# Kernel tuning notes

Hardware: AMD Instinct MI355X
Metric: run time of the kernel (lower is better)

## Reference

```python
import jax, jax.numpy as jnp
import numpy as np

N = 100000
E = 1600000
IN_FEATS = 512
N_CLASSES = 40
H1, D1 = 8, 8
H2, D2 = 1, N_CLASSES


def gat_conv(x, src, dst, W, al, ar, b, H, D):
    # x: [N, F] -> h: [N, H, D]
    n = x.shape[0]
    h = (x @ W).reshape(n, H, D)
    el = (h * al[None]).sum(-1)  # [N, H]
    er = (h * ar[None]).sum(-1)  # [N, H]
    e = jax.nn.leaky_relu(el[src] + er[dst], 0.2)  # [E, H]
    # segment softmax over destination neighborhoods
    emax = jax.ops.segment_max(e, dst, num_segments=n)  # [N, H]
    ee = jnp.exp(e - emax[dst])
    denom = jax.ops.segment_sum(ee, dst, num_segments=n)  # [N, H]
    a = ee / (denom[dst] + 1e-9)  # [E, H]
    m = h[src] * a[:, :, None]  # [E, H, D]
    out = jax.ops.segment_sum(m, dst, num_segments=n)  # [N, H, D]
    return out + b.reshape(1, H, D)


def setup_inputs() -> dict:
    key = jax.random.key(0)
    ks = jax.random.split(key, 12)
    g1 = 1.0 / np.sqrt(IN_FEATS)
    g2 = 1.0 / np.sqrt(H1 * D1)
    return {
        "x": jax.random.normal(ks[0], (N, IN_FEATS), jnp.float32),
        "src": jax.random.randint(ks[1], (E,), 0, N, jnp.int32),
        "dst": jax.random.randint(ks[2], (E,), 0, N, jnp.int32),
        "W1": jax.random.normal(ks[3], (IN_FEATS, H1 * D1), jnp.float32) * g1,
        "al1": jax.random.normal(ks[4], (H1, D1), jnp.float32) * 0.1,
        "ar1": jax.random.normal(ks[5], (H1, D1), jnp.float32) * 0.1,
        "b1": jnp.zeros((H1 * D1,), jnp.float32),
        "W2": jax.random.normal(ks[6], (H1 * D1, H2 * D2), jnp.float32) * g2,
        "al2": jax.random.normal(ks[7], (H2, D2), jnp.float32) * 0.1,
        "ar2": jax.random.normal(ks[8], (H2, D2), jnp.float32) * 0.1,
        "b2": jnp.zeros((H2 * D2,), jnp.float32),
    }


def reference(x, src, dst, W1, al1, ar1, b1, W2, al2, ar2, b2):
    h = gat_conv(x, src, dst, W1, al1, ar1, b1, H1, D1)  # [N, 8, 8]
    h = jax.nn.elu(h.reshape(N, H1 * D1))  # [N, 64]
    h = gat_conv(h, src, dst, W2, al2, ar2, b2, H2, D2).mean(axis=1)  # [N, n_classes]
    return jax.nn.log_softmax(h, axis=1)
```

## Files before the change

kernel.cpp:

```cpp
#include <hip/hip_runtime.h>
#include <hip/hip_bf16.h>
#include <math.h>

#define NCLS 40
#define H2S 64
#define PWG 256
#define BSH 9
#define NBMAX 512
#define SRCB 23
#define CSRCAP 14336

typedef __attribute__((ext_vector_type(8))) short bf16x8;
typedef __attribute__((ext_vector_type(4))) float f32x4;

__device__ inline float bf2f(ushort u) {
    unsigned v = ((unsigned)u) << 16;
    float f;
    __builtin_memcpy(&f, &v, 4);
    return f;
}
__device__ inline ushort f2bf(float f) {
    unsigned v;
    __builtin_memcpy(&v, &f, 4);
    unsigned r = (v + 0x7FFFu + ((v >> 16) & 1u)) >> 16;
    return (ushort)r;
}
__device__ inline unsigned pkbf(float a, float b) {
    unsigned ua, ub;
    __builtin_memcpy(&ua, &a, 4);
    __builtin_memcpy(&ub, &b, 4);
    return __builtin_amdgcn_perm(ub + 0x8000u, ua + 0x8000u, 0x07060302u);
}

__global__ __launch_bounds__(256) void hist_prep_kernel(
    const int* __restrict__ dst, int* __restrict__ hist, int Ee, int chunk, int NB,
    const float* __restrict__ W1, ushort* __restrict__ W1t,
    const float* __restrict__ W2, const float* __restrict__ al2,
    const float* __restrict__ ar2, float* __restrict__ wal2,
    float* __restrict__ war2)
{
    if (blockIdx.x >= PWG) {
        int bb = blockIdx.x - PWG;
        if (bb < 128) {
            int id = bb * 256 + threadIdx.x;
            int k = id >> 6, c = id & 63;
            W1t[c * 512 + k] = f2bf(W1[k * 64 + c]);
        } else if (threadIdx.x < 64) {
            int k = threadIdx.x;
            float a = 0.f, b = 0.f;
            for (int c = 0; c < NCLS; c++) {
                float w = W2[k * NCLS + c];
                a += w * al2[c];
                b += w * ar2[c];
            }
            wal2[k] = a;
            war2[k] = b;
        }
        return;
    }
    __shared__ int lh[256];
    const int wg = blockIdx.x, tid = threadIdx.x;
    lh[tid] = 0;
    __syncthreads();
    const int beg = wg * chunk;
    const int endv = min(Ee, beg + chunk);
#pragma unroll 4
    for (int i = beg + tid; i < endv; i += 256) atomicAdd(&lh[dst[i] >> BSH], 1);
    __syncthreads();
    if (tid < NB) hist[tid * PWG + wg] = lh[tid];
}

__global__ __launch_bounds__(256) void scanA_kernel(int* __restrict__ hist,
                                                    int* __restrict__ bucketTot)
{
    __shared__ int s[256];
    const int b = blockIdx.x, tid = threadIdx.x;
    int v = hist[b * PWG + tid];
    s[tid] = v;
    __syncthreads();
#pragma unroll
    for (int o = 1; o < 256; o <<= 1) {
        int t = (tid >= o) ? s[tid - o] : 0;
        __syncthreads();
        s[tid] += t;
        __syncthreads();
    }
    hist[b * PWG + tid] = s[tid] - v;
    if (tid == 255) bucketTot[b] = s[255];
}

__global__ __launch_bounds__(256) void part_gemm1_kernel(
    const int* __restrict__ src, const int* __restrict__ dst,
    const int* __restrict__ hist, const int* __restrict__ bucketTot,
    unsigned* __restrict__ ebuf, int Ee, int chunk, int NB,
    const float* __restrict__ x, const ushort* __restrict__ W1t,
    const float* __restrict__ al1, const float* __restrict__ ar1,
    ushort* __restrict__ h1b, float* __restrict__ el1,
    float* __restrict__ er1, int Nn)
{
    __shared__ ushort As[64 * 72];
    __shared__ ushort Bs[64 * 72];

    if (blockIdx.x < PWG) {
        int* cur = (int*)As;
        int* stmp = (int*)Bs;
        const int wg = blockIdx.x, tid = threadIdx.x;
        int v = (tid < NB) ? bucketTot[tid] : 0;
        stmp[tid] = v;
        __syncthreads();
#pragma unroll
        for (int o = 1; o < 256; o <<= 1) {
            int t = (tid >= o) ? stmp[tid - o] : 0;
            __syncthreads();
            stmp[tid] += t;
            __syncthreads();
        }
        if (tid < NB) cur[tid] = hist[tid * PWG + wg] + (stmp[tid] - v);
        __syncthreads();
        const int beg = wg * chunk;
        const int endv = min(Ee, beg + chunk);
        for (int i = beg + tid; i < endv; i += 256) {
            int d = dst[i];
            int p = atomicAdd(&cur[d >> BSH], 1);
            ebuf[p] = ((unsigned)(d & ((1 << BSH) - 1)) << SRCB) | (unsigned)src[i];
        }
        return;
    }

    const int t = threadIdx.x;
    const int lane = t & 63, w = t >> 6;
    const int tile = (blockIdx.x - PWG) * 64;

    f32x4 acc[4] = {};

    const int sr = t >> 2;
    const int sk = (t & 3) * 16;
    const int arow = tile + sr;
    const bool rowok = arow < Nn;
    const float* xrow = x + (size_t)arow * 512;
    const ushort* wrow = W1t + (size_t)sr * 512;

    const int r = lane & 15, g = lane >> 4;

    float4 f0 = make_float4(0.f, 0.f, 0.f, 0.f), f1 = f0, f2 = f0, f3 = f0;
    bf16x8 bv0, bv1;
    if (rowok) {
        f0 = *(const float4*)(xrow + sk);
        f1 = *(const float4*)(xrow + sk + 4);
        f2 = *(const float4*)(xrow + sk + 8);
        f3 = *(const float4*)(xrow + sk + 12);
    }
    bv0 = *(const bf16x8*)(wrow + sk);
    bv1 = *(const bf16x8*)(wrow + sk + 8);

    for (int k0 = 0; k0 < 512; k0 += 64) {
        uint4 aw0, aw1;
        aw0.x = pkbf(f0.x, f0.y); aw0.y = pkbf(f0.z, f0.w);
        aw0.z = pkbf(f1.x, f1.y); aw0.w = pkbf(f1.z, f1.w);
        aw1.x = pkbf(f2.x, f2.y); aw1.y = pkbf(f2.z, f2.w);
        aw1.z = pkbf(f3.x, f3.y); aw1.w = pkbf(f3.z, f3.w);
        *(uint4*)&As[sr * 72 + sk] = aw0;
        *(uint4*)&As[sr * 72 + sk + 8] = aw1;
        *(bf16x8*)&Bs[sr * 72 + sk] = bv0;
        *(bf16x8*)&Bs[sr * 72 + sk + 8] = bv1;
        __syncthreads();

        int k1 = k0 + 64;
        if (k1 < 512) {
            if (rowok) {
                f0 = *(const float4*)(xrow + k1 + sk);
                f1 = *(const float4*)(xrow + k1 + sk + 4);
                f2 = *(const float4*)(xrow + k1 + sk + 8);
                f3 = *(const float4*)(xrow + k1 + sk + 12);
            }
            bv0 = *(const bf16x8*)(wrow + k1 + sk);
            bv1 = *(const bf16x8*)(wrow + k1 + sk + 8);
        }

        bf16x8 af0 = *(const bf16x8*)&As[(w * 16 + r) * 72 + g * 8];
        bf16x8 af1 = *(const bf16x8*)&As[(w * 16 + r) * 72 + 32 + g * 8];
#pragma unroll
        for (int cb = 0; cb < 4; cb++) {
            bf16x8 bf0 = *(const bf16x8*)&Bs[(cb * 16 + r) * 72 + g * 8];
            acc[cb] = __builtin_amdgcn_mfma_f32_16x16x32_bf16(af0, bf0, acc[cb], 0, 0, 0);
        }
#pragma unroll
        for (int cb = 0; cb < 4; cb++) {
            bf16x8 bf1 = *(const bf16x8*)&Bs[(cb * 16 + r) * 72 + 32 + g * 8];
            acc[cb] = __builtin_amdgcn_mfma_f32_16x16x32_bf16(af1, bf1, acc[cb], 0, 0, 0);
        }
        __syncthreads();
    }

    float alv[4], arv[4];
#pragma unroll
    for (int cb = 0; cb < 4; cb++) {
        alv[cb] = al1[cb * 16 + r];
        arv[cb] = ar1[cb * 16 + r];
    }
#pragma unroll
    for (int v = 0; v < 4; v++) {
        int row = tile + w * 16 + g * 4 + v;
        bool ok = row < Nn;
#pragma unroll
        for (int cb = 0; cb < 4; cb++) {
            if (ok) h1b[(size_t)row * 64 + cb * 16 + r] = f2bf(acc[cb][v]);
            float pel = acc[cb][v] * alv[cb];
            float per = acc[cb][v] * arv[cb];
            pel += __shfl_xor(pel, 1); per += __shfl_xor(per, 1);
            pel += __shfl_xor(pel, 2); per += __shfl_xor(per, 2);
            pel += __shfl_xor(pel, 4); per += __shfl_xor(per, 4);
            if (ok && (r & 7) == 0) {
                int head = cb * 2 + (r >> 3);
                el1[row * 8 + head] = pel;
                er1[row * 8 + head] = per;
            }
        }
    }
}

__global__ __launch_bounds__(512) void bucket_csr_kernel(const unsigned* __restrict__ ebuf,
                                                         const int* __restrict__ bucketTot,
                                                         int* __restrict__ row_start,
                                                         int* __restrict__ perm_src,
                                                         int Nn, int Ee, int NB)
{
    __shared__ unsigned stage[CSRCAP];
    __shared__ int cnt[512];
    __shared__ int s[512];
    __shared__ int cur[512];
    __shared__ int bt[256];
    const int b = blockIdx.x, tid = threadIdx.x;
    const int base = b << BSH;

    if (tid < 256) bt[tid] = (tid < NB) ? bucketTot[tid] : 0;
    __syncthreads();
#pragma unroll
    for (int o = 1; o < 256; o <<= 1) {
        int t = (tid >= o && tid < 256) ? bt[tid - o] : 0;
        __syncthreads();
        if (tid < 256) bt[tid] += t;
        __syncthreads();
    }
    const int be = bt[b];
    const int bb = be - bucketTot[b];
    const int m = be - bb;

    cnt[tid] = 0;
    __syncthreads();
    for (int idx = tid; idx < m; idx += 512) {
        unsigned pk = ebuf[bb + idx];
        if (idx < CSRCAP) stage[idx] = pk;
        atomicAdd(&cnt[pk >> SRCB], 1);
    }
    __syncthreads();
    int v = cnt[tid];
    s[tid] = v;
    __syncthreads();
#pragma unroll
    for (int o = 1; o < 512; o <<= 1) {
        int t = (tid >= o) ? s[tid - o] : 0;
        __syncthreads();
        s[tid] += t;
        __syncthreads();
    }
    const int off = bb + s[tid] - v;
    const int node = base + tid;
    if (node < Nn) row_start[node] = off;
    cur[tid] = off;
    __syncthreads();
    for (int idx = tid; idx < m; idx += 512) {
        unsigned pk = (idx < CSRCAP) ? stage[idx] : ebuf[bb + idx];
        int p = atomicAdd(&cur[pk >> SRCB], 1);
        perm_src[p] = (int)(pk & ((1u << SRCB) - 1u));
    }
    if (b == NB - 1 && tid == 0) row_start[Nn] = Ee;
}

__global__ __launch_bounds__(256) void agg1_kernel(
    const ushort* __restrict__ h1b, const float* __restrict__ el1,
    const float* __restrict__ er1, const int* __restrict__ row_start,
    const int* __restrict__ perm_src, const float* __restrict__ b1,
    ushort* __restrict__ hmidb, int Nn)
{
    const int wid = (blockIdx.x * blockDim.x + threadIdx.x) >> 6;
    const int lane = threadIdx.x & 63;
    if (wid >= Nn) return;
    const int g = lane >> 4;
    const int q = lane & 15;
    const int h = q >> 1;
    const int beg = row_start[wid], end = row_start[wid + 1];
    const float er = er1[wid * 8 + h];

    float a0 = 0.f, a1 = 0.f, a2 = 0.f, a3 = 0.f, denom = 0.f;
    for (int i0 = beg; i0 < end; i0 += 64) {
        const int cnt = min(end - i0, 64);
        int pv = (i0 + lane < end) ? perm_src[i0 + lane] : 0;
        for (int j = 0; j < cnt; j += 16) {
            const int e0 = j + g, e1 = j + 4 + g, e2 = j + 8 + g, e3 = j + 12 + g;
            const int s0 = __shfl(pv, min(e0, cnt - 1));
            const int s1 = __shfl(pv, min(e1, cnt - 1));
            const int s2 = __shfl(pv, min(e2, cnt - 1));
            const int s3 = __shfl(pv, min(e3, cnt - 1));
            ushort4 r0 = *(const ushort4*)&h1b[(size_t)s0 * 64 + q * 4];
            ushort4 r1 = *(const ushort4*)&h1b[(size_t)s1 * 64 + q * 4];
            ushort4 r2 = *(const ushort4*)&h1b[(size_t)s2 * 64 + q * 4];
            ushort4 r3 = *(const ushort4*)&h1b[(size_t)s3 * 64 + q * 4];
            float x0 = el1[s0 * 8 + h];
            float x1 = el1[s1 * 8 + h];
            float x2 = el1[s2 * 8 + h];
            float x3 = el1[s3 * 8 + h];
            float e;
            e = x0 + er; e = (e >= 0.f) ? e : 0.2f * e;
            float w0 = (e0 < cnt) ? __expf(e) : 0.f;
            e = x1 + er; e = (e >= 0.f) ? e : 0.2f * e;
            float w1 = (e1 < cnt) ? __expf(e) : 0.f;
            e = x2 + er; e = (e >= 0.f) ? e : 0.2f * e;
            float w2 = (e2 < cnt) ? __expf(e) : 0.f;
            e = x3 + er; e = (e >= 0.f) ? e : 0.2f * e;
            float w3 = (e3 < cnt) ? __expf(e) : 0.f;
            denom += (w0 + w1) + (w2 + w3);
            a0 += bf2f(r0.x) * w0 + bf2f(r1.x) * w1 + bf2f(r2.x) * w2 + bf2f(r3.x) * w3;
            a1 += bf2f(r0.y) * w0 + bf2f(r1.y) * w1 + bf2f(r2.y) * w2 + bf2f(r3.y) * w3;
            a2 += bf2f(r0.z) * w0 + bf2f(r1.z) * w1 + bf2f(r2.z) * w2 + bf2f(r3.z) * w3;
            a3 += bf2f(r0.w) * w0 + bf2f(r1.w) * w1 + bf2f(r2.w) * w2 + bf2f(r3.w) * w3;
        }
    }
    denom += __shfl_xor(denom, 16); denom += __shfl_xor(denom, 32);
    a0 += __shfl_xor(a0, 16); a0 += __shfl_xor(a0, 32);
    a1 += __shfl_xor(a1, 16); a1 += __shfl_xor(a1, 32);
    a2 += __shfl_xor(a2, 16); a2 += __shfl_xor(a2, 32);
    a3 += __shfl_xor(a3, 16); a3 += __shfl_xor(a3, 32);
    if (g == 0) {
        const float4 bv = *(const float4*)&b1[q * 4];
        const float inv = 1.f / (denom + 1e-9f);
        float v0 = a0 * inv + bv.x;
        float v1 = a1 * inv + bv.y;
        float v2 = a2 * inv + bv.z;
        float v3 = a3 * inv + bv.w;
        v0 = (v0 > 0.f) ? v0 : expm1f(v0);
        v1 = (v1 > 0.f) ? v1 : expm1f(v1);
        v2 = (v2 > 0.f) ? v2 : expm1f(v2);
        v3 = (v3 > 0.f) ? v3 : expm1f(v3);
        uint2 o;
        o.x = pkbf(v0, v1);
        o.y = pkbf(v2, v3);
        *(uint2*)&hmidb[(size_t)wid * 64 + q * 4] = o;
    }
}

__global__ __launch_bounds__(256) void gemm2_kernel(
    const ushort* __restrict__ hmidb, const float* __restrict__ W2,
    const float* __restrict__ wal2, const float* __restrict__ war2,
    ushort* __restrict__ h2b, int Nn)
{
    __shared__ float w2s[64 * NCLS];
    __shared__ float wals[64], wars[64];
    for (int i = threadIdx.x; i < 64 * NCLS; i += blockDim.x) w2s[i] = W2[i];
    if (threadIdx.x < 64) {
        wals[threadIdx.x] = wal2[threadIdx.x];
        wars[threadIdx.x] = war2[threadIdx.x];
    }
    __syncthreads();
    int n = blockIdx.x * blockDim.x + threadIdx.x;
    if (n >= Nn) return;

    float out[NCLS];
#pragma unroll
    for (int c = 0; c < NCLS; c++) out[c] = 0.f;
    float accel = 0.f, accer = 0.f;

#pragma unroll 4
    for (int k4 = 0; k4 < 16; k4++) {
        ushort4 u = *(const ushort4*)&hmidb[(size_t)n * 64 + k4 * 4];
        float h0 = bf2f(u.x), h1 = bf2f(u.y), h2 = bf2f(u.z), h3 = bf2f(u.w);
        accel += h0 * wals[k4 * 4] + h1 * wals[k4 * 4 + 1] + h2 * wals[k4 * 4 + 2] + h3 * wals[k4 * 4 + 3];
        accer += h0 * wars[k4 * 4] + h1 * wars[k4 * 4 + 1] + h2 * wars[k4 * 4 + 2] + h3 * wars[k4 * 4 + 3];
#pragma unroll
        for (int c = 0; c < NCLS; c++) {
            out[c] += h0 * w2s[(k4 * 4 + 0) * NCLS + c] + h1 * w2s[(k4 * 4 + 1) * NCLS + c] +
                      h2 * w2s[(k4 * 4 + 2) * NCLS + c] + h3 * w2s[(k4 * 4 + 3) * NCLS + c];
        }
    }
    ushort* row = h2b + (size_t)n * H2S;
#pragma unroll
    for (int c = 0; c < NCLS; c += 2) {
        *(unsigned*)&row[c] = pkbf(out[c], out[c + 1]);
    }
    ((float*)row)[20] = accel;
    ((float*)row)[21] = accer;
}

__global__ __launch_bounds__(256) void agg2_kernel(
    const ushort* __restrict__ h2b, const int* __restrict__ row_start,
    const int* __restrict__ perm_src, const float* __restrict__ b2,
    float* __restrict__ out, int Nn)
{
    const int wid = (blockIdx.x * blockDim.x + threadIdx.x) >> 6;
    const int lane = threadIdx.x & 63;
    if (wid >= Nn) return;
    const int g = lane >> 4;
    const int q = lane & 15;
    const int beg = row_start[wid], end = row_start[wid + 1];
    const float er = ((const float*)(h2b + (size_t)wid * H2S))[21];

    float a0 = 0.f, a1 = 0.f, a2 = 0.f, a3 = 0.f, denom = 0.f;
    for (int i0 = beg; i0 < end; i0 += 64) {
        const int cnt = min(end - i0, 64);
        int pv = (i0 + lane < end) ? perm_src[i0 + lane] : 0;
        for (int j = 0; j < cnt; j += 16) {
            const int e0 = j + g, e1 = j + 4 + g, e2 = j + 8 + g, e3 = j + 12 + g;
            const int s0 = __shfl(pv, min(e0, cnt - 1));
            const int s1 = __shfl(pv, min(e1, cnt - 1));
            const int s2 = __shfl(pv, min(e2, cnt - 1));
            const int s3 = __shfl(pv, min(e3, cnt - 1));
            const ushort* rp0 = h2b + (size_t)s0 * H2S;
            const ushort* rp1 = h2b + (size_t)s1 * H2S;
            const ushort* rp2 = h2b + (size_t)s2 * H2S;
            const ushort* rp3 = h2b + (size_t)s3 * H2S;
            ushort4 r0 = *(const ushort4*)(rp0 + q * 4);
            ushort4 r1 = *(const ushort4*)(rp1 + q * 4);
            ushort4 r2 = *(const ushort4*)(rp2 + q * 4);
            ushort4 r3 = *(const ushort4*)(rp3 + q * 4);
            float x0 = ((const float*)rp0)[20];
            float x1 = ((const float*)rp1)[20];
            float x2 = ((const float*)rp2)[20];
            float x3 = ((const float*)rp3)[20];
            float e;
            e = x0 + er; e = (e >= 0.f) ? e : 0.2f * e;
            float w0 = (e0 < cnt) ? __expf(e) : 0.f;
            e = x1 + er; e = (e >= 0.f) ? e : 0.2f * e;
            float w1 = (e1 < cnt) ? __expf(e) : 0.f;
            e = x2 + er; e = (e >= 0.f) ? e : 0.2f * e;
            float w2 = (e2 < cnt) ? __expf(e) : 0.f;
            e = x3 + er; e = (e >= 0.f) ? e : 0.2f * e;
            float w3 = (e3 < cnt) ? __expf(e) : 0.f;
            denom += (w0 + w1) + (w2 + w3);
            a0 += bf2f(r0.x) * w0 + bf2f(r1.x) * w1 + bf2f(r2.x) * w2 + bf2f(r3.x) * w3;
            a1 += bf2f(r0.y) * w0 + bf2f(r1.y) * w1 + bf2f(r2.y) * w2 + bf2f(r3.y) * w3;
            a2 += bf2f(r0.z) * w0 + bf2f(r1.z) * w1 + bf2f(r2.z) * w2 + bf2f(r3.z) * w3;
            a3 += bf2f(r0.w) * w0 + bf2f(r1.w) * w1 + bf2f(r2.w) * w2 + bf2f(r3.w) * w3;
        }
    }
    denom += __shfl_xor(denom, 16); denom += __shfl_xor(denom, 32);
    a0 += __shfl_xor(a0, 16); a0 += __shfl_xor(a0, 32);
    a1 += __shfl_xor(a1, 16); a1 += __shfl_xor(a1, 32);
    a2 += __shfl_xor(a2, 16); a2 += __shfl_xor(a2, 32);
    a3 += __shfl_xor(a3, 16); a3 += __shfl_xor(a3, 32);

    const bool act = (g == 0) && (q < 10);
    float v0, v1, v2, v3;
    if (act) {
        const float4 bv = *(const float4*)&b2[q * 4];
        const float inv = 1.f / (denom + 1e-9f);
        v0 = a0 * inv + bv.x;
        v1 = a1 * inv + bv.y;
        v2 = a2 * inv + bv.z;
        v3 = a3 * inv + bv.w;
    } else {
        v0 = v1 = v2 = v3 = -1e30f;
    }
    float mx = fmaxf(fmaxf(v0, v1), fmaxf(v2, v3));
#pragma unroll
    for (int o = 1; o < 64; o <<= 1) mx = fmaxf(mx, __shfl_xor(mx, o));
    float sx = act ? (__expf(v0 - mx) + __expf(v1 - mx) + __expf(v2 - mx) + __expf(v3 - mx)) : 0.f;
#pragma unroll
    for (int o = 1; o < 64; o <<= 1) sx += __shfl_xor(sx, o);
    if (act) {
        float lg = mx + __logf(sx);
        float4 o4 = make_float4(v0 - lg, v1 - lg, v2 - lg, v3 - lg);
        *(float4*)&out[(size_t)wid * NCLS + q * 4] = o4;
    }
}

extern "C" void kernel_launch(void* const* d_in, const int* in_sizes, int n_in,
                              void* d_out, int out_size, void* d_ws, size_t ws_size,
                              hipStream_t stream)
{
    const float* x   = (const float*)d_in[0];
    const int*   src = (const int*)d_in[1];
    const int*   dst = (const int*)d_in[2];
    const float* W1  = (const float*)d_in[3];
    const float* al1 = (const float*)d_in[4];
    const float* ar1 = (const float*)d_in[5];
    const float* b1  = (const float*)d_in[6];
    const float* W2  = (const float*)d_in[7];
    const float* al2 = (const float*)d_in[8];
    const float* ar2 = (const float*)d_in[9];
    const float* b2  = (const float*)d_in[10];
    float* out = (float*)d_out;

    const int Nn = in_sizes[0] / 512;
    const int Ee = in_sizes[1];
    const int NB = (Nn + (1 << BSH) - 1) >> BSH;
    const int chunk = (Ee + PWG - 1) / PWG;

    char* wsb = (char*)d_ws;
    size_t off = 0;
    auto alloc = [&](size_t bytes) -> void* {
        off = (off + 15) & ~(size_t)15;
        void* p = wsb + off;
        off += bytes;
        return p;
    };
    ushort* h1b   = (ushort*)alloc((size_t)Nn * 64 * 2);
    ushort* hmidb = (ushort*)alloc((size_t)Nn * 64 * 2);
    ushort* h2b   = (ushort*)alloc((size_t)Nn * H2S * 2);
    ushort* W1t   = (ushort*)alloc(64 * 512 * 2);
    float* el1  = (float*)alloc((size_t)Nn * 8 * 4);
    float* er1  = (float*)alloc((size_t)Nn * 8 * 4);
    float* wal2 = (float*)alloc(64 * 4);
    float* war2 = (float*)alloc(64 * 4);
    int* row_start  = (int*)alloc((size_t)(Nn + 1) * 4);
    int* hist       = (int*)alloc((size_t)NB * PWG * 4);
    int* bucketTot  = (int*)alloc((size_t)NB * 4);
    int* perm_src   = (int*)alloc((size_t)Ee * 4);
    unsigned* ebuf  = (unsigned*)alloc((size_t)Ee * 4);

    hist_prep_kernel<<<PWG + 129, 256, 0, stream>>>(dst, hist, Ee, chunk, NB,
                                                    W1, W1t, W2, al2, ar2, wal2, war2);
    scanA_kernel<<<NB, 256, 0, stream>>>(hist, bucketTot);
    part_gemm1_kernel<<<PWG + (Nn + 63) / 64, 256, 0, stream>>>(
        src, dst, hist, bucketTot, ebuf, Ee, chunk, NB,
        x, W1t, al1, ar1, h1b, el1, er1, Nn);
    bucket_csr_kernel<<<NB, 512, 0, stream>>>(ebuf, bucketTot, row_start, perm_src, Nn, Ee, NB);

    agg1_kernel<<<(Nn + 3) / 4, 256, 0, stream>>>(h1b, el1, er1, row_start, perm_src, b1, hmidb, Nn);

    gemm2_kernel<<<(Nn + 255) / 256, 256, 0, stream>>>(hmidb, W2, wal2, war2, h2b, Nn);
    agg2_kernel<<<(Nn + 3) / 4, 256, 0, stream>>>(h2b, row_start, perm_src, b2, out, Nn);
}
```

Baseline: 223.5 us.

## Load GEMM1 MFMA operands directly from global memory, dropping LDS staging

The fused partition+GEMM1 kernel no longer stages x and W1 tiles through shared memory with barriers. Each lane now loads its own A-fragment rows from x and its B-fragments from W1t directly into registers, packs them to bf16 and issues the MFMAs. This removes the LDS writes, LDS reads and __syncthreads per k-step, and shrinks the kernel's shared-memory footprint to the partition path's needs. In exchange, W1t is re-read by every wave from global/L2 and the x loads are less coalesced, since each lane reads 32-byte pieces of separate rows.

Result: slower. 261.0 us (+16.8%).

```diff
diff --git a/kernel.cpp b/kernel.cpp
--- a/kernel.cpp
+++ b/kernel.cpp
@@ -98,12 +98,10 @@
     ushort* __restrict__ h1b, float* __restrict__ el1,
     float* __restrict__ er1, int Nn)
 {
-    __shared__ ushort As[64 * 72];
-    __shared__ ushort Bs[64 * 72];
+    __shared__ int cur[NBMAX];
+    __shared__ int stmp[256];
 
     if (blockIdx.x < PWG) {
-        int* cur = (int*)As;
-        int* stmp = (int*)Bs;
         const int wg = blockIdx.x, tid = threadIdx.x;
         int v = (tid < NB) ? bucketTot[tid] : 0;
         stmp[tid] = v;
@@ -130,66 +128,41 @@
     const int t = threadIdx.x;
     const int lane = t & 63, w = t >> 6;
     const int tile = (blockIdx.x - PWG) * 64;
+    const int r = lane & 15, g = lane >> 4;
+
+    const int row = tile + w * 16 + r;
+    const int rowc = min(row, Nn - 1);
+    const float* xrow = x + (size_t)rowc * 512 + g * 8;
+    const ushort* wbase = W1t + g * 8;
 
     f32x4 acc[4] = {};
 
-    const int sr = t >> 2;
-    const int sk = (t & 3) * 16;
-    const int arow = tile + sr;
-    const bool rowok = arow < Nn;
-    const float* xrow = x + (size_t)arow * 512;
-    const ushort* wrow = W1t + (size_t)sr * 512;
-
-    const int r = lane & 15, g = lane >> 4;
-
-    float4 f0 = make_float4(0.f, 0.f, 0.f, 0.f), f1 = f0, f2 = f0, f3 = f0;
-    bf16x8 bv0, bv1;
-    if (rowok) {
-        f0 = *(const float4*)(xrow + sk);
-        f1 = *(const float4*)(xrow + sk + 4);
-        f2 = *(const float4*)(xrow + sk + 8);
-        f3 = *(const float4*)(xrow + sk + 12);
-    }
-    bv0 = *(const bf16x8*)(wrow + sk);
-    bv1 = *(const bf16x8*)(wrow + sk + 8);
-
+#pragma unroll 2
     for (int k0 = 0; k0 < 512; k0 += 64) {
-        uint4 aw0, aw1;
-        aw0.x = pkbf(f0.x, f0.y); aw0.y = pkbf(f0.z, f0.w);
-        aw0.z = pkbf(f1.x, f1.y); aw0.w = pkbf(f1.z, f1.w);
-        aw1.x = pkbf(f2.x, f2.y); aw1.y = pkbf(f2.z, f2.w);
-        aw1.z = pkbf(f3.x, f3.y); aw1.w = pkbf(f3.z, f3.w);
-        *(uint4*)&As[sr * 72 + sk] = aw0;
-        *(uint4*)&As[sr * 72 + sk + 8] = aw1;
-        *(bf16x8*)&Bs[sr * 72 + sk] = bv0;
-        *(bf16x8*)&Bs[sr * 72 + sk + 8] = bv1;
-        __syncthreads();
-
-        int k1 = k0 + 64;
-        if (k1 < 512) {
-            if (rowok) {
-                f0 = *(const float4*)(xrow + k1 + sk);
-                f1 = *(const float4*)(xrow + k1 + sk + 4);
-                f2 = *(const float4*)(xrow + k1 + sk + 8);
-                f3 = *(const float4*)(xrow + k1 + sk + 12);
-            }
-            bv0 = *(const bf16x8*)(wrow + k1 + sk);
-            bv1 = *(const bf16x8*)(wrow + k1 + sk + 8);
-        }
-
-        bf16x8 af0 = *(const bf16x8*)&As[(w * 16 + r) * 72 + g * 8];
-        bf16x8 af1 = *(const bf16x8*)&As[(w * 16 + r) * 72 + 32 + g * 8];
+        float4 fA0 = *(const float4*)(xrow + k0);
+        float4 fA1 = *(const float4*)(xrow + k0 + 4);
+        float4 fA2 = *(const float4*)(xrow + k0 + 32);
+        float4 fA3 = *(const float4*)(xrow + k0 + 36);
+        bf16x8 bf0[4], bf1[4];
 #pragma unroll
         for (int cb = 0; cb < 4; cb++) {
-            bf16x8 bf0 = *(const bf16x8*)&Bs[(cb * 16 + r) * 72 + g * 8];
-            acc[cb] = __builtin_amdgcn_mfma_f32_16x16x32_bf16(af0, bf0, acc[cb], 0, 0, 0);
-        }
-#pragma unroll
-        for (int cb = 0; cb < 4; cb++) {
-            bf16x8 bf1 = *(const bf16x8*)&Bs[(cb * 16 + r) * 72 + 32 + g * 8];
-            acc[cb] = __builtin_amdgcn_mfma_f32_16x16x32_bf16(af1, bf1, acc[cb], 0, 0, 0);
-        }
-        __syncthreads();
+            bf0[cb] = *(const bf16x8*)(wbase + (cb * 16 + r) * 512 + k0);
+            bf1[cb] = *(const bf16x8*)(wbase + (cb * 16 + r) * 512 + k0 + 32);
+        }
+        uint4 a0w, a1w;
+        a0w.x = pkbf(fA0.x, fA0.y); a0w.y = pkbf(fA0.z, fA0.w);
+        a0w.z = pkbf(fA1.x, fA1.y); a0w.w = pkbf(fA1.z, fA1.w);
+        a1w.x = pkbf(fA2.x, fA2.y); a1w.y = pkbf(fA2.z, fA2.w);
+        a1w.z = pkbf(fA3.x, fA3.y); a1w.w = pkbf(fA3.z, fA3.w);
+        bf16x8 af0, af1;
+        __builtin_memcpy(&af0, &a0w, 16);
+        __builtin_memcpy(&af1, &a1w, 16);
+#pragma unroll
+        for (int cb = 0; cb < 4; cb++)
+            acc[cb] = __builtin_amdgcn_mfma_f32_16x16x32_bf16(af0, bf0[cb], acc[cb], 0, 0, 0);
+#pragma unroll
+        for (int cb = 0; cb < 4; cb++)
+            acc[cb] = __builtin_amdgcn_mfma_f32_16x16x32_bf16(af1, bf1[cb], acc[cb], 0, 0, 0);
     }
 
     float alv[4], arv[4];
@@ -200,11 +173,11 @@
     }
 #pragma unroll
     for (int v = 0; v < 4; v++) {
-        int row = tile + w * 16 + g * 4 + v;
-        bool ok = row < Nn;
+        int orow = tile + w * 16 + g * 4 + v;
+        bool ok = orow < Nn;
 #pragma unroll
         for (int cb = 0; cb < 4; cb++) {
-            if (ok) h1b[(size_t)row * 64 + cb * 16 + r] = f2bf(acc[cb][v]);
+            if (ok) h1b[(size_t)orow * 64 + cb * 16 + r] = f2bf(acc[cb][v]);
             float pel = acc[cb][v] * alv[cb];
             float per = acc[cb][v] * arv[cb];
             pel += __shfl_xor(pel, 1); per += __shfl_xor(per, 1);
@@ -212,8 +185,8 @@
             pel += __shfl_xor(pel, 4); per += __shfl_xor(per, 4);
             if (ok && (r & 7) == 0) {
                 int head = cb * 2 + (r >> 3);
-                el1[row * 8 + head] = pel;
-                er1[row * 8 + head] = per;
+                el1[orow * 8 + head] = pel;
+                er1[orow * 8 + head] = per;
             }
         }
     }
```
